# Performance work log

Hardware: AMD Instinct MI355X
Metric: run time of the kernel (lower is better)

Reference implementation:

```python
import jax, jax.numpy as jnp
import numpy as np

NUM_HEADS = 16
ALPHA = 1.0          # attention_logits_alpha
SOFTCAP = 50.0       # logit_softcapping


def setup_inputs() -> dict:
    key = jax.random.key(0)
    ks = jax.random.split(key, 7)
    B, S, E = 2, 2048, 2048
    mk = lambda k, shape, sc=1.0: jax.random.normal(k, shape, dtype=jnp.float32) * sc
    return {
        "q": mk(ks[0], (B, S, E)),
        "k": mk(ks[1], (B, S, E)),
        "v": mk(ks[2], (B, S, E)),
        # nn.Linear weights are [out, in]; xavier-ish scale 1/sqrt(E)
        "Wq": mk(ks[3], (E, E), E ** -0.5),
        "Wk": mk(ks[4], (E, E), E ** -0.5),
        "Wv": mk(ks[5], (E, E), E ** -0.5),
        "Wo": mk(ks[6], (E, E), E ** -0.5),
    }


def reference(q, k, v, Wq, Wk, Wv, Wo):
    B, S, E = q.shape
    H = NUM_HEADS
    D = E // H  # head_dim = 128

    def split_heads(x):  # [B,S,E] -> [B,H,S,D]
        return x.reshape(B, S, H, D).transpose(0, 2, 1, 3)

    qh = split_heads(q @ Wq.T)  # q_projection_scale = 1.0
    kh = split_heads(k @ Wk.T)
    vh = split_heads(v @ Wv.T)

    # scaled_dot_product: scale q by 1/sqrt(head_dim)
    qh = qh * (D ** -0.5)
    logits = ALPHA * jnp.einsum("bhqd,bhkd->bhqk", qh, kh)
    # logit softcapping: cap * tanh(logits / cap)
    logits = SOFTCAP * jnp.tanh(logits / SOFTCAP)
    # fp32 softmax (softmax_dtype_fp32=True)
    probs = jax.nn.softmax(logits.astype(jnp.float32), axis=-1).astype(qh.dtype)
    # dropout rate 0.0 -> identity
    ctx = jnp.einsum("bhqk,bhkd->bhqd", probs, vh)
    ctx = ctx.transpose(0, 2, 1, 3).reshape(B, S, E)
    return ctx @ Wo.T  # output_projection_scale = 1.0
```

## Files before the change

kernel.cpp:

```cpp
#include <hip/hip_runtime.h>
#include <hip/hip_bf16.h>
#include <stdint.h>


typedef __attribute__((ext_vector_type(8))) short s16x8;
typedef __attribute__((ext_vector_type(4))) short s16x4;
typedef __attribute__((ext_vector_type(4))) float f32x4;

typedef const __attribute__((address_space(1))) char* gcptr;
typedef __attribute__((address_space(3))) char* lcptr;

#define MFMA_BF16(a, b, c) __builtin_amdgcn_mfma_f32_16x16x32_bf16((a), (b), (c), 0, 0, 0)

__device__ __forceinline__ short f2bf(float f) {
  union { float f; unsigned u; } x; x.f = f;
  unsigned r = (x.u + 0x7fffu + ((x.u >> 16) & 1u)) >> 16;
  return (short)r;
}

__device__ __forceinline__ void gload16(const void* g, void* lds) {
  __builtin_amdgcn_global_load_lds((gcptr)g, (lcptr)lds, 16, 0, 0);
}

constexpr int GM = 4096, GN = 2048, GK = 2048;
constexpr int SL = 2048, EMB = 2048, HD = 128;

__global__ void cvt_bf16(const float* __restrict__ in, short* __restrict__ out,
                         int n8) {
  int i = blockIdx.x * blockDim.x + threadIdx.x;
  int stride = gridDim.x * blockDim.x;
  for (; i < n8; i += stride) {
    f32x4 a = *reinterpret_cast<const f32x4*>(in + (size_t)i * 8);
    f32x4 b = *reinterpret_cast<const f32x4*>(in + (size_t)i * 8 + 4);
    s16x8 w;
#pragma unroll
    for (int j = 0; j < 4; ++j) { w[j] = f2bf(a[j]); w[4 + j] = f2bf(b[j]); }
    *reinterpret_cast<s16x8*>(out + (size_t)i * 8) = w;
  }
}

template <bool OF32>
__global__ __launch_bounds__(256, 2)
void gemm_bt_bf16(const short* __restrict__ A, const short* __restrict__ B,
                  void* __restrict__ Cv) {
  __shared__ __align__(16) short As[128 * 64];
  __shared__ __align__(16) short Bs[128 * 64];
  const int tid = threadIdx.x;
  const int lane = tid & 63;
  const int wid = tid >> 6;
  const int wr = wid >> 1, wc = wid & 1;
  const int g = lane >> 4, r = lane & 15;
  const int bm = blockIdx.y, bn = blockIdx.x;

  const f32x4 fz = {0.f, 0.f, 0.f, 0.f};
  f32x4 acc[4][4];
#pragma unroll
  for (int m = 0; m < 4; ++m)
#pragma unroll
    for (int n = 0; n < 4; ++n) acc[m][n] = fz;

  const short* Ab = A + (size_t)bm * 128 * GK;
  const short* Bb = B + (size_t)bn * 128 * GK;

  for (int kt = 0; kt < GK; kt += 64) {
#pragma unroll
    for (int i = 0; i < 4; ++i) {
      int c = i * 256 + tid;
      int row = c >> 3, c8 = c & 7;
      gload16(Ab + (size_t)row * GK + kt + c8 * 8, As + c * 8);
      gload16(Bb + (size_t)row * GK + kt + c8 * 8, Bs + c * 8);
    }
    __syncthreads();
#pragma unroll
    for (int kk = 0; kk < 2; ++kk) {
      s16x8 af[4], bf[4];
#pragma unroll
      for (int m = 0; m < 4; ++m)
        af[m] = *reinterpret_cast<const s16x8*>(As + (wr * 64 + m * 16 + r) * 64 + kk * 32 + g * 8);
#pragma unroll
      for (int n = 0; n < 4; ++n)
        bf[n] = *reinterpret_cast<const s16x8*>(Bs + (wc * 64 + n * 16 + r) * 64 + kk * 32 + g * 8);
#pragma unroll
      for (int m = 0; m < 4; ++m)
#pragma unroll
        for (int n = 0; n < 4; ++n) acc[m][n] = MFMA_BF16(af[m], bf[n], acc[m][n]);
    }
    __syncthreads();
  }

#pragma unroll
  for (int m = 0; m < 4; ++m)
#pragma unroll
    for (int j = 0; j < 4; ++j) {
      int crow = bm * 128 + wr * 64 + m * 16 + g * 4 + j;
      size_t off = (size_t)crow * GN + bn * 128 + wc * 64 + r;
#pragma unroll
      for (int n = 0; n < 4; ++n) {
        if constexpr (OF32) ((float*)Cv)[off + n * 16] = acc[m][n][j];
        else                ((short*)Cv)[off + n * 16] = f2bf(acc[m][n][j]);
      }
    }
}

template <bool AF32, bool BF32, bool OF32>
__global__ __launch_bounds__(256, 2)
void gemm_bt(const void* __restrict__ Av, const void* __restrict__ Bv,
             void* __restrict__ Cv) {
  __shared__ __align__(16) short As[128 * 64];
  __shared__ __align__(16) short Bs[128 * 64];
  const int tid = threadIdx.x;
  const int lane = tid & 63;
  const int wid = tid >> 6;
  const int wr = wid >> 1, wc = wid & 1;
  const int g = lane >> 4, r = lane & 15;
  const int bm = blockIdx.y, bn = blockIdx.x;

  const f32x4 fz = {0.f, 0.f, 0.f, 0.f};
  f32x4 acc[4][4];
#pragma unroll
  for (int m = 0; m < 4; ++m)
#pragma unroll
    for (int n = 0; n < 4; ++n) acc[m][n] = fz;

  const float* Afp = (const float*)Av + (size_t)bm * 128 * GK;
  const short* Abf = (const short*)Av + (size_t)bm * 128 * GK;
  const float* Bfp = (const float*)Bv + (size_t)bn * 128 * GK;
  const short* Bbf = (const short*)Bv + (size_t)bn * 128 * GK;

  for (int kt = 0; kt < GK; kt += 64) {
    f32x4 raf[8], rbf[8];
    s16x8 rab[4], rbb[4];
    if constexpr (AF32) {
#pragma unroll
      for (int i = 0; i < 8; ++i) {
        int c = i * 256 + tid, row = c >> 4, ch = c & 15;
        raf[i] = *reinterpret_cast<const f32x4*>(Afp + (size_t)row * GK + kt + ch * 4);
      }
    } else {
#pragma unroll
      for (int i = 0; i < 4; ++i) {
        int c = i * 256 + tid, row = c >> 3, ch = c & 7;
        rab[i] = *reinterpret_cast<const s16x8*>(Abf + (size_t)row * GK + kt + ch * 8);
      }
    }
    if constexpr (BF32) {
#pragma unroll
      for (int i = 0; i < 8; ++i) {
        int c = i * 256 + tid, row = c >> 4, ch = c & 15;
        rbf[i] = *reinterpret_cast<const f32x4*>(Bfp + (size_t)row * GK + kt + ch * 4);
      }
    } else {
#pragma unroll
      for (int i = 0; i < 4; ++i) {
        int c = i * 256 + tid, row = c >> 3, ch = c & 7;
        rbb[i] = *reinterpret_cast<const s16x8*>(Bbf + (size_t)row * GK + kt + ch * 8);
      }
    }
    __syncthreads();
    if constexpr (AF32) {
#pragma unroll
      for (int i = 0; i < 8; ++i) {
        int c = i * 256 + tid;
        s16x4 w;
#pragma unroll
        for (int j = 0; j < 4; ++j) w[j] = f2bf(raf[i][j]);
        *reinterpret_cast<s16x4*>(As + c * 4) = w;
      }
    } else {
#pragma unroll
      for (int i = 0; i < 4; ++i)
        *reinterpret_cast<s16x8*>(As + (i * 256 + tid) * 8) = rab[i];
    }
    if constexpr (BF32) {
#pragma unroll
      for (int i = 0; i < 8; ++i) {
        int c = i * 256 + tid;
        s16x4 w;
#pragma unroll
        for (int j = 0; j < 4; ++j) w[j] = f2bf(rbf[i][j]);
        *reinterpret_cast<s16x4*>(Bs + c * 4) = w;
      }
    } else {
#pragma unroll
      for (int i = 0; i < 4; ++i)
        *reinterpret_cast<s16x8*>(Bs + (i * 256 + tid) * 8) = rbb[i];
    }
    __syncthreads();

#pragma unroll
    for (int kk = 0; kk < 2; ++kk) {
      s16x8 af[4], bf[4];
#pragma unroll
      for (int m = 0; m < 4; ++m)
        af[m] = *reinterpret_cast<const s16x8*>(As + (wr * 64 + m * 16 + r) * 64 + kk * 32 + g * 8);
#pragma unroll
      for (int n = 0; n < 4; ++n)
        bf[n] = *reinterpret_cast<const s16x8*>(Bs + (wc * 64 + n * 16 + r) * 64 + kk * 32 + g * 8);
#pragma unroll
      for (int m = 0; m < 4; ++m)
#pragma unroll
        for (int n = 0; n < 4; ++n) acc[m][n] = MFMA_BF16(af[m], bf[n], acc[m][n]);
    }
  }

#pragma unroll
  for (int m = 0; m < 4; ++m)
#pragma unroll
    for (int j = 0; j < 4; ++j) {
      int crow = bm * 128 + wr * 64 + m * 16 + g * 4 + j;
      size_t off = (size_t)crow * GN + bn * 128 + wc * 64 + r;
#pragma unroll
      for (int n = 0; n < 4; ++n) {
        if constexpr (OF32) ((float*)Cv)[off + n * 16] = acc[m][n][j];
        else                ((short*)Cv)[off + n * 16] = f2bf(acc[m][n][j]);
      }
    }
}

__global__ __launch_bounds__(256, 2)
void attn(const short* __restrict__ Q, const short* __restrict__ K,
          const short* __restrict__ V, short* __restrict__ O) {
  __shared__ __align__(16) short Ks[64 * 136];
  __shared__ __align__(16) short Vt[128 * 72];
  __shared__ __align__(16) short Ps[4][2][16 * 72];

  const int tid = threadIdx.x;
  const int lane = tid & 63;
  const int wid = tid >> 6;
  const int g = lane >> 4, r = lane & 15;
  const int qb = blockIdx.x;
  const int bh = blockIdx.y;
  const int b = bh >> 4, h = bh & 15;
  const size_t base = (size_t)b * SL * EMB + (size_t)h * HD;

  const int q0 = qb * 128 + wid * 32;
  s16x8 qf[2][4];
#pragma unroll
  for (int s = 0; s < 2; ++s)
#pragma unroll
    for (int kk = 0; kk < 4; ++kk)
      qf[s][kk] = *reinterpret_cast<const s16x8*>(
          Q + base + (size_t)(q0 + s * 16 + r) * EMB + kk * 32 + g * 8);

  const f32x4 fz = {0.f, 0.f, 0.f, 0.f};
  float l_run[2][4];
  f32x4 acc_o[2][8];
#pragma unroll
  for (int s = 0; s < 2; ++s) {
#pragma unroll
    for (int i = 0; i < 4; ++i) l_run[s][i] = 0.f;
#pragma unroll
    for (int i = 0; i < 8; ++i) acc_o[s][i] = fz;
  }

  const float SCALE = 0.08838834764831845f;
  const float C50I = 0.02f;
  const float CA = -1.f / 3.f, CB = 2.f / 15.f;

  const int rr0 = tid >> 4, c8 = tid & 15;
  s16x8 kreg[4], vreg[4];
#pragma unroll
  for (int i = 0; i < 4; ++i) {
    int rr = rr0 + i * 16;
    kreg[i] = *reinterpret_cast<const s16x8*>(K + base + (size_t)rr * EMB + c8 * 8);
    vreg[i] = *reinterpret_cast<const s16x8*>(V + base + (size_t)rr * EMB + c8 * 8);
  }

  for (int t = 0; t < SL / 64; ++t) {
    __syncthreads();
    const int colswb = ((c8 & 7) << 3);
#pragma unroll
    for (int i = 0; i < 4; ++i) {
      int rr = rr0 + i * 16;
      *reinterpret_cast<s16x8*>(&Ks[rr * 136 + c8 * 8]) = kreg[i];
      int colsw = rr ^ colswb;
#pragma unroll
      for (int j = 0; j < 8; ++j) Vt[(c8 * 8 + j) * 72 + colsw] = vreg[i][j];
    }
    __syncthreads();

    if (t + 1 < SL / 64) {
      const int kv1 = (t + 1) * 64;
#pragma unroll
      for (int i = 0; i < 4; ++i) {
        int rr = rr0 + i * 16;
        kreg[i] = *reinterpret_cast<const s16x8*>(K + base + (size_t)(kv1 + rr) * EMB + c8 * 8);
        vreg[i] = *reinterpret_cast<const s16x8*>(V + base + (size_t)(kv1 + rr) * EMB + c8 * 8);
      }
    }

    f32x4 sv[2][4];
#pragma unroll
    for (int kn = 0; kn < 4; ++kn) {
      sv[0][kn] = fz; sv[1][kn] = fz;
#pragma unroll
      for (int kk = 0; kk < 4; ++kk) {
        s16x8 kf = *reinterpret_cast<const s16x8*>(&Ks[(kn * 16 + r) * 136 + kk * 32 + g * 8]);
        sv[0][kn] = MFMA_BF16(qf[0][kk], kf, sv[0][kn]);
        sv[1][kn] = MFMA_BF16(qf[1][kk], kf, sv[1][kn]);
      }
    }

#pragma unroll
    for (int s = 0; s < 2; ++s)
#pragma unroll
      for (int kn = 0; kn < 4; ++kn)
#pragma unroll
        for (int reg = 0; reg < 4; ++reg) {
          float z = sv[s][kn][reg] * SCALE;
          float x = z * C50I;
          float x2 = x * x;
          float poly = __builtin_fmaf(x2, __builtin_fmaf(x2, CB, CA), 1.f);
          float cap = fminf(z * poly, 50.f);
          float pe = __expf(cap - 50.f);
          l_run[s][reg] += pe;
          sv[s][kn][reg] = pe;
        }

#pragma unroll
    for (int s = 0; s < 2; ++s)
#pragma unroll
      for (int kn = 0; kn < 4; ++kn)
#pragma unroll
        for (int reg = 0; reg < 4; ++reg)
          Ps[wid][s][(g * 4 + reg) * 72 + kn * 16 + r] = f2bf(sv[s][kn][reg]);

#pragma unroll
    for (int c = 0; c < 2; ++c) {
      s16x8 pa0 = *reinterpret_cast<const s16x8*>(&Ps[wid][0][r * 72 + c * 32 + g * 8]);
      s16x8 pa1 = *reinterpret_cast<const s16x8*>(&Ps[wid][1][r * 72 + c * 32 + g * 8]);
#pragma unroll
      for (int dn = 0; dn < 8; ++dn) {
        int d = dn * 16 + r;
        int e = ((dn * 2) + (r >> 3)) & 7;
        s16x8 vf = *reinterpret_cast<const s16x8*>(&Vt[d * 72 + (((c * 4 + g) ^ e) * 8)]);
        acc_o[0][dn] = MFMA_BF16(pa0, vf, acc_o[0][dn]);
        acc_o[1][dn] = MFMA_BF16(pa1, vf, acc_o[1][dn]);
      }
    }
  }

#pragma unroll
  for (int s = 0; s < 2; ++s) {
#pragma unroll
    for (int reg = 0; reg < 4; ++reg) {
#pragma unroll
      for (int off = 1; off < 16; off <<= 1)
        l_run[s][reg] += __shfl_xor(l_run[s][reg], off);
      l_run[s][reg] = 1.f / l_run[s][reg];
    }
#pragma unroll
    for (int dn = 0; dn < 8; ++dn)
#pragma unroll
      for (int reg = 0; reg < 4; ++reg) {
        int row = q0 + s * 16 + g * 4 + reg;
        O[base + (size_t)row * EMB + dn * 16 + r] = f2bf(acc_o[s][dn][reg] * l_run[s][reg]);
      }
  }
}

__global__ void fill_f32(float* p, int n, float val) {
  int i = blockIdx.x * blockDim.x + threadIdx.x;
  if (i < n) p[i] = val;
}

extern "C" void kernel_launch(void* const* d_in, const int* in_sizes, int n_in,
                              void* d_out, int out_size, void* d_ws, size_t ws_size,
                              hipStream_t stream) {
  const float* q  = (const float*)d_in[0];
  const float* k  = (const float*)d_in[1];
  const float* v  = (const float*)d_in[2];
  const float* wq = (const float*)d_in[3];
  const float* wk = (const float*)d_in[4];
  const float* wv = (const float*)d_in[5];
  const float* wo = (const float*)d_in[6];
  float* out = (float*)d_out;

  bool ok = (n_in == 7) && out_size == 8388608;
  for (int i = 0; i < 3 && ok; ++i) ok = (in_sizes[i] == 8388608);
  for (int i = 3; i < 7 && ok; ++i) ok = (in_sizes[i] == 4194304);
  if (!ok) {
    fill_f32<<<(out_size + 255) / 256, 256, 0, stream>>>(out, out_size, 150.f);
    return;
  }

  const size_t NA = 8388608;
  const size_t NW = 4194304;
  const size_t NE = (size_t)GM * GN;
  const size_t need_small = 4 * NE * sizeof(short);
  const size_t need_big = (3 * NA + 4 * NW + 4 * NE) * sizeof(short);
  if (ws_size < need_small) {
    fill_f32<<<(out_size + 255) / 256, 256, 0, stream>>>(out, out_size, 128.f);
    return;
  }

  dim3 blk(256);
  dim3 gg(GN / 128, GM / 128);
  dim3 ga(SL / 128, 32);

  if (ws_size >= need_big) {
    short* bq  = (short*)d_ws;
    short* bk  = bq + NA;
    short* bv  = bk + NA;
    short* bwq = bv + NA;
    short* bwk = bwq + NW;
    short* bwv = bwk + NW;
    short* bwo = bwv + NW;
    short* Qp  = bwo + NW;
    short* Kp  = Qp + NE;
    short* Vp  = Kp + NE;
    short* Cx  = Vp + NE;

    cvt_bf16<<<2048, 256, 0, stream>>>(q,  bq,  (int)(NA / 8));
    cvt_bf16<<<2048, 256, 0, stream>>>(k,  bk,  (int)(NA / 8));
    cvt_bf16<<<2048, 256, 0, stream>>>(v,  bv,  (int)(NA / 8));
    cvt_bf16<<<1024, 256, 0, stream>>>(wq, bwq, (int)(NW / 8));
    cvt_bf16<<<1024, 256, 0, stream>>>(wk, bwk, (int)(NW / 8));
    cvt_bf16<<<1024, 256, 0, stream>>>(wv, bwv, (int)(NW / 8));
    cvt_bf16<<<1024, 256, 0, stream>>>(wo, bwo, (int)(NW / 8));

    gemm_bt_bf16<false><<<gg, blk, 0, stream>>>(bq, bwq, Qp);
    gemm_bt_bf16<false><<<gg, blk, 0, stream>>>(bk, bwk, Kp);
    gemm_bt_bf16<false><<<gg, blk, 0, stream>>>(bv, bwv, Vp);
    attn<<<ga, blk, 0, stream>>>(Qp, Kp, Vp, Cx);
    gemm_bt_bf16<true><<<gg, blk, 0, stream>>>(Cx, bwo, out);
  } else {
    short* Qp = (short*)d_ws;
    short* Kp = Qp + NE;
    short* Vp = Kp + NE;
    short* Cx = Vp + NE;
    gemm_bt<true, true, false><<<gg, blk, 0, stream>>>(q, wq, Qp);
    gemm_bt<true, true, false><<<gg, blk, 0, stream>>>(k, wk, Kp);
    gemm_bt<true, true, false><<<gg, blk, 0, stream>>>(v, wv, Vp);
    attn<<<ga, blk, 0, stream>>>(Qp, Kp, Vp, Cx);
    gemm_bt<false, true, true><<<gg, blk, 0, stream>>>(Cx, wo, out);
  }
}
```

Measured before the change: 360.4 us.

## Halve attention KV tile to 32 for higher occupancy, fuse conversions into one kernel

The attention kernel now processes 32 keys per iteration instead of 64. Its LDS buffers and register arrays shrink accordingly, and launch bounds are raised to allow 4 blocks per CU, aiming to improve latency hiding. The seven separate fp32-to-bf16 conversion launches are merged into one kernel that writes into the contiguous workspace, and the fallback fp32-input GEMM path is removed. The smaller tile doubles the number of loop iterations and barriers, and a too-small workspace now gets the error fill instead of the fallback.

```diff
diff --git a/kernel.cpp b/kernel.cpp
--- a/kernel.cpp
+++ b/kernel.cpp
@@ -25,17 +25,33 @@
 constexpr int GM = 4096, GN = 2048, GK = 2048;
 constexpr int SL = 2048, EMB = 2048, HD = 128;
 
-__global__ void cvt_bf16(const float* __restrict__ in, short* __restrict__ out,
-                         int n8) {
+__global__ void cvt_all(const float* __restrict__ q, const float* __restrict__ k,
+                        const float* __restrict__ v, const float* __restrict__ wq,
+                        const float* __restrict__ wk, const float* __restrict__ wv,
+                        const float* __restrict__ wo, short* __restrict__ dst) {
+  const int N8A = 1 << 20, N8W = 1 << 19;
+  const int total = 3 * N8A + 4 * N8W;
   int i = blockIdx.x * blockDim.x + threadIdx.x;
   int stride = gridDim.x * blockDim.x;
-  for (; i < n8; i += stride) {
-    f32x4 a = *reinterpret_cast<const f32x4*>(in + (size_t)i * 8);
-    f32x4 b = *reinterpret_cast<const f32x4*>(in + (size_t)i * 8 + 4);
-    s16x8 w;
-#pragma unroll
-    for (int j = 0; j < 4; ++j) { w[j] = f2bf(a[j]); w[4 + j] = f2bf(b[j]); }
-    *reinterpret_cast<s16x8*>(out + (size_t)i * 8) = w;
+  for (; i < total; i += stride) {
+    const float* src;
+    size_t loc;
+    if (i < 3 * N8A) {
+      int sel = i >> 20;
+      loc = (size_t)(i & (N8A - 1));
+      src = sel == 0 ? q : (sel == 1 ? k : v);
+    } else {
+      int w = i - 3 * N8A;
+      int sel = w >> 19;
+      loc = (size_t)(w & (N8W - 1));
+      src = sel == 0 ? wq : (sel == 1 ? wk : (sel == 2 ? wv : wo));
+    }
+    f32x4 a = *reinterpret_cast<const f32x4*>(src + loc * 8);
+    f32x4 b = *reinterpret_cast<const f32x4*>(src + loc * 8 + 4);
+    s16x8 w8;
+#pragma unroll
+    for (int j = 0; j < 4; ++j) { w8[j] = f2bf(a[j]); w8[4 + j] = f2bf(b[j]); }
+    *reinterpret_cast<s16x8*>(dst + (size_t)i * 8) = w8;
   }
 }
 
@@ -102,127 +118,12 @@
     }
 }
 
-template <bool AF32, bool BF32, bool OF32>
-__global__ __launch_bounds__(256, 2)
-void gemm_bt(const void* __restrict__ Av, const void* __restrict__ Bv,
-             void* __restrict__ Cv) {
-  __shared__ __align__(16) short As[128 * 64];
-  __shared__ __align__(16) short Bs[128 * 64];
-  const int tid = threadIdx.x;
-  const int lane = tid & 63;
-  const int wid = tid >> 6;
-  const int wr = wid >> 1, wc = wid & 1;
-  const int g = lane >> 4, r = lane & 15;
-  const int bm = blockIdx.y, bn = blockIdx.x;
-
-  const f32x4 fz = {0.f, 0.f, 0.f, 0.f};
-  f32x4 acc[4][4];
-#pragma unroll
-  for (int m = 0; m < 4; ++m)
-#pragma unroll
-    for (int n = 0; n < 4; ++n) acc[m][n] = fz;
-
-  const float* Afp = (const float*)Av + (size_t)bm * 128 * GK;
-  const short* Abf = (const short*)Av + (size_t)bm * 128 * GK;
-  const float* Bfp = (const float*)Bv + (size_t)bn * 128 * GK;
-  const short* Bbf = (const short*)Bv + (size_t)bn * 128 * GK;
-
-  for (int kt = 0; kt < GK; kt += 64) {
-    f32x4 raf[8], rbf[8];
-    s16x8 rab[4], rbb[4];
-    if constexpr (AF32) {
-#pragma unroll
-      for (int i = 0; i < 8; ++i) {
-        int c = i * 256 + tid, row = c >> 4, ch = c & 15;
-        raf[i] = *reinterpret_cast<const f32x4*>(Afp + (size_t)row * GK + kt + ch * 4);
-      }
-    } else {
-#pragma unroll
-      for (int i = 0; i < 4; ++i) {
-        int c = i * 256 + tid, row = c >> 3, ch = c & 7;
-        rab[i] = *reinterpret_cast<const s16x8*>(Abf + (size_t)row * GK + kt + ch * 8);
-      }
-    }
-    if constexpr (BF32) {
-#pragma unroll
-      for (int i = 0; i < 8; ++i) {
-        int c = i * 256 + tid, row = c >> 4, ch = c & 15;
-        rbf[i] = *reinterpret_cast<const f32x4*>(Bfp + (size_t)row * GK + kt + ch * 4);
-      }
-    } else {
-#pragma unroll
-      for (int i = 0; i < 4; ++i) {
-        int c = i * 256 + tid, row = c >> 3, ch = c & 7;
-        rbb[i] = *reinterpret_cast<const s16x8*>(Bbf + (size_t)row * GK + kt + ch * 8);
-      }
-    }
-    __syncthreads();
-    if constexpr (AF32) {
-#pragma unroll
-      for (int i = 0; i < 8; ++i) {
-        int c = i * 256 + tid;
-        s16x4 w;
-#pragma unroll
-        for (int j = 0; j < 4; ++j) w[j] = f2bf(raf[i][j]);
-        *reinterpret_cast<s16x4*>(As + c * 4) = w;
-      }
-    } else {
-#pragma unroll
-      for (int i = 0; i < 4; ++i)
-        *reinterpret_cast<s16x8*>(As + (i * 256 + tid) * 8) = rab[i];
-    }
-    if constexpr (BF32) {
-#pragma unroll
-      for (int i = 0; i < 8; ++i) {
-        int c = i * 256 + tid;
-        s16x4 w;
-#pragma unroll
-        for (int j = 0; j < 4; ++j) w[j] = f2bf(rbf[i][j]);
-        *reinterpret_cast<s16x4*>(Bs + c * 4) = w;
-      }
-    } else {
-#pragma unroll
-      for (int i = 0; i < 4; ++i)
-        *reinterpret_cast<s16x8*>(Bs + (i * 256 + tid) * 8) = rbb[i];
-    }
-    __syncthreads();
-
-#pragma unroll
-    for (int kk = 0; kk < 2; ++kk) {
-      s16x8 af[4], bf[4];
-#pragma unroll
-      for (int m = 0; m < 4; ++m)
-        af[m] = *reinterpret_cast<const s16x8*>(As + (wr * 64 + m * 16 + r) * 64 + kk * 32 + g * 8);
-#pragma unroll
-      for (int n = 0; n < 4; ++n)
-        bf[n] = *reinterpret_cast<const s16x8*>(Bs + (wc * 64 + n * 16 + r) * 64 + kk * 32 + g * 8);
-#pragma unroll
-      for (int m = 0; m < 4; ++m)
-#pragma unroll
-        for (int n = 0; n < 4; ++n) acc[m][n] = MFMA_BF16(af[m], bf[n], acc[m][n]);
-    }
-  }
-
-#pragma unroll
-  for (int m = 0; m < 4; ++m)
-#pragma unroll
-    for (int j = 0; j < 4; ++j) {
-      int crow = bm * 128 + wr * 64 + m * 16 + g * 4 + j;
-      size_t off = (size_t)crow * GN + bn * 128 + wc * 64 + r;
-#pragma unroll
-      for (int n = 0; n < 4; ++n) {
-        if constexpr (OF32) ((float*)Cv)[off + n * 16] = acc[m][n][j];
-        else                ((short*)Cv)[off + n * 16] = f2bf(acc[m][n][j]);
-      }
-    }
-}
-
-__global__ __launch_bounds__(256, 2)
+__global__ __launch_bounds__(256, 4)
 void attn(const short* __restrict__ Q, const short* __restrict__ K,
           const short* __restrict__ V, short* __restrict__ O) {
-  __shared__ __align__(16) short Ks[64 * 136];
-  __shared__ __align__(16) short Vt[128 * 72];
-  __shared__ __align__(16) short Ps[4][2][16 * 72];
+  __shared__ __align__(16) short Ks[32 * 136];
+  __shared__ __align__(16) short Vt[128 * 40];
+  __shared__ __align__(16) short Ps[4][2][16 * 36];
 
   const int tid = threadIdx.x;
   const int lane = tid & 63;
@@ -258,40 +159,40 @@
   const float CA = -1.f / 3.f, CB = 2.f / 15.f;
 
   const int rr0 = tid >> 4, c8 = tid & 15;
-  s16x8 kreg[4], vreg[4];
-#pragma unroll
-  for (int i = 0; i < 4; ++i) {
+  s16x8 kreg[2], vreg[2];
+#pragma unroll
+  for (int i = 0; i < 2; ++i) {
     int rr = rr0 + i * 16;
     kreg[i] = *reinterpret_cast<const s16x8*>(K + base + (size_t)rr * EMB + c8 * 8);
     vreg[i] = *reinterpret_cast<const s16x8*>(V + base + (size_t)rr * EMB + c8 * 8);
   }
 
-  for (int t = 0; t < SL / 64; ++t) {
+  for (int t = 0; t < SL / 32; ++t) {
     __syncthreads();
-    const int colswb = ((c8 & 7) << 3);
-#pragma unroll
-    for (int i = 0; i < 4; ++i) {
+    const int colswb = (c8 & 3) << 3;
+#pragma unroll
+    for (int i = 0; i < 2; ++i) {
       int rr = rr0 + i * 16;
       *reinterpret_cast<s16x8*>(&Ks[rr * 136 + c8 * 8]) = kreg[i];
       int colsw = rr ^ colswb;
 #pragma unroll
-      for (int j = 0; j < 8; ++j) Vt[(c8 * 8 + j) * 72 + colsw] = vreg[i][j];
+      for (int j = 0; j < 8; ++j) Vt[(c8 * 8 + j) * 40 + colsw] = vreg[i][j];
     }
     __syncthreads();
 
-    if (t + 1 < SL / 64) {
-      const int kv1 = (t + 1) * 64;
-#pragma unroll
-      for (int i = 0; i < 4; ++i) {
+    if (t + 1 < SL / 32) {
+      const int kv1 = (t + 1) * 32;
+#pragma unroll
+      for (int i = 0; i < 2; ++i) {
         int rr = rr0 + i * 16;
         kreg[i] = *reinterpret_cast<const s16x8*>(K + base + (size_t)(kv1 + rr) * EMB + c8 * 8);
         vreg[i] = *reinterpret_cast<const s16x8*>(V + base + (size_t)(kv1 + rr) * EMB + c8 * 8);
       }
     }
 
-    f32x4 sv[2][4];
-#pragma unroll
-    for (int kn = 0; kn < 4; ++kn) {
+    f32x4 sv[2][2];
+#pragma unroll
+    for (int kn = 0; kn < 2; ++kn) {
       sv[0][kn] = fz; sv[1][kn] = fz;
 #pragma unroll
       for (int kk = 0; kk < 4; ++kk) {
@@ -304,7 +205,7 @@
 #pragma unroll
     for (int s = 0; s < 2; ++s)
 #pragma unroll
-      for (int kn = 0; kn < 4; ++kn)
+      for (int kn = 0; kn < 2; ++kn)
 #pragma unroll
         for (int reg = 0; reg < 4; ++reg) {
           float z = sv[s][kn][reg] * SCALE;
@@ -320,20 +221,19 @@
 #pragma unroll
     for (int s = 0; s < 2; ++s)
 #pragma unroll
-      for (int kn = 0; kn < 4; ++kn)
+      for (int kn = 0; kn < 2; ++kn)
 #pragma unroll
         for (int reg = 0; reg < 4; ++reg)
-          Ps[wid][s][(g * 4 + reg) * 72 + kn * 16 + r] = f2bf(sv[s][kn][reg]);
-
-#pragma unroll
-    for (int c = 0; c < 2; ++c) {
-      s16x8 pa0 = *reinterpret_cast<const s16x8*>(&Ps[wid][0][r * 72 + c * 32 + g * 8]);
-      s16x8 pa1 = *reinterpret_cast<const s16x8*>(&Ps[wid][1][r * 72 + c * 32 + g * 8]);
+          Ps[wid][s][(g * 4 + reg) * 36 + kn * 16 + r] = f2bf(sv[s][kn][reg]);
+
+    {
+      s16x8 pa0 = *reinterpret_cast<const s16x8*>(&Ps[wid][0][r * 36 + g * 8]);
+      s16x8 pa1 = *reinterpret_cast<const s16x8*>(&Ps[wid][1][r * 36 + g * 8]);
 #pragma unroll
       for (int dn = 0; dn < 8; ++dn) {
         int d = dn * 16 + r;
-        int e = ((dn * 2) + (r >> 3)) & 7;
-        s16x8 vf = *reinterpret_cast<const s16x8*>(&Vt[d * 72 + (((c * 4 + g) ^ e) * 8)]);
+        int e = ((dn * 2) + (r >> 3)) & 3;
+        s16x8 vf = *reinterpret_cast<const s16x8*>(&Vt[d * 40 + ((g ^ e) * 8)]);
         acc_o[0][dn] = MFMA_BF16(pa0, vf, acc_o[0][dn]);
         acc_o[1][dn] = MFMA_BF16(pa1, vf, acc_o[1][dn]);
       }
@@ -387,52 +287,33 @@
   const size_t NA = 8388608;
   const size_t NW = 4194304;
   const size_t NE = (size_t)GM * GN;
-  const size_t need_small = 4 * NE * sizeof(short);
-  const size_t need_big = (3 * NA + 4 * NW + 4 * NE) * sizeof(short);
-  if (ws_size < need_small) {
+  const size_t need = (3 * NA + 4 * NW + 4 * NE) * sizeof(short);
+  if (ws_size < need) {
     fill_f32<<<(out_size + 255) / 256, 256, 0, stream>>>(out, out_size, 128.f);
     return;
   }
+
+  short* bq  = (short*)d_ws;
+  short* bk  = bq + NA;
+  short* bv  = bk + NA;
+  short* bwq = bv + NA;
+  short* bwk = bwq + NW;
+  short* bwv = bwk + NW;
+  short* bwo = bwv + NW;
+  short* Qp  = bwo + NW;
+  short* Kp  = Qp + NE;
+  short* Vp  = Kp + NE;
+  short* Cx  = Vp + NE;
 
   dim3 blk(256);
   dim3 gg(GN / 128, GM / 128);
   dim3 ga(SL / 128, 32);
 
-  if (ws_size >= need_big) {
-    short* bq  = (short*)d_ws;
-    short* bk  = bq + NA;
-    short* bv  = bk + NA;
-    short* bwq = bv + NA;
-    short* bwk = bwq + NW;
-    short* bwv = bwk + NW;
-    short* bwo = bwv + NW;
-    short* Qp  = bwo + NW;
-    short* Kp  = Qp + NE;
-    short* Vp  = Kp + NE;
-    short* Cx  = Vp + NE;
-
-    cvt_bf16<<<2048, 256, 0, stream>>>(q,  bq,  (int)(NA / 8));
-    cvt_bf16<<<2048, 256, 0, stream>>>(k,  bk,  (int)(NA / 8));
-    cvt_bf16<<<2048, 256, 0, stream>>>(v,  bv,  (int)(NA / 8));
-    cvt_bf16<<<1024, 256, 0, stream>>>(wq, bwq, (int)(NW / 8));
-    cvt_bf16<<<1024, 256, 0, stream>>>(wk, bwk, (int)(NW / 8));
-    cvt_bf16<<<1024, 256, 0, stream>>>(wv, bwv, (int)(NW / 8));
-    cvt_bf16<<<1024, 256, 0, stream>>>(wo, bwo, (int)(NW / 8));
-
-    gemm_bt_bf16<false><<<gg, blk, 0, stream>>>(bq, bwq, Qp);
-    gemm_bt_bf16<false><<<gg, blk, 0, stream>>>(bk, bwk, Kp);
-    gemm_bt_bf16<false><<<gg, blk, 0, stream>>>(bv, bwv, Vp);
-    attn<<<ga, blk, 0, stream>>>(Qp, Kp, Vp, Cx);
-    gemm_bt_bf16<true><<<gg, blk, 0, stream>>>(Cx, bwo, out);
-  } else {
-    short* Qp = (short*)d_ws;
-    short* Kp = Qp + NE;
-    short* Vp = Kp + NE;
-    short* Cx = Vp + NE;
-    gemm_bt<true, true, false><<<gg, blk, 0, stream>>>(q, wq, Qp);
-    gemm_bt<true, true, false><<<gg, blk, 0, stream>>>(k, wk, Kp);
-    gemm_bt<true, true, false><<<gg, blk, 0, stream>>>(v, wv, Vp);
-    attn<<<ga, blk, 0, stream>>>(Qp, Kp, Vp, Cx);
-    gemm_bt<false, true, true><<<gg, blk, 0, stream>>>(Cx, wo, out);
-  }
-}
+  cvt_all<<<2048, 256, 0, stream>>>(q, k, v, wq, wk, wv, wo, bq);
+
+  gemm_bt_bf16<false><<<gg, blk, 0, stream>>>(bq, bwq, Qp);
+  gemm_bt_bf16<false><<<gg, blk, 0, stream>>>(bk, bwk, Kp);
+  gemm_bt_bf16<false><<<gg, blk, 0, stream>>>(bv, bwv, Vp);
+  attn<<<ga, blk, 0, stream>>>(Qp, Kp, Vp, Cx);
+  gemm_bt_bf16<true><<<gg, blk, 0, stream>>>(Cx, bwo, out);
+}
```

Result: slower. 441.4 us (+22.5%).
